# Performance work log

Hardware: AMD Instinct MI355X
Metric: run time of the kernel (lower is better)

Reference implementation:

```python
import jax, jax.numpy as jnp
import numpy as np

HEADS = 16
HEAD_SIZE = 64
INF = 1e12  # bert4keras K.infinity() uses a large finite value


def _rotate_interleaved(x):
    # result[..., 2i] = -x[..., 2i+1]; result[..., 2i+1] = x[..., 2i]
    x2 = jnp.stack([-x[..., 1::2], x[..., ::2]], axis=-1)
    return x2.reshape(x.shape)


def setup_inputs() -> dict:
    key = jax.random.key(0)
    k1, k2 = jax.random.split(key)
    B, N, D = 8, 1024, 1024
    x = jax.random.normal(k1, (B, N, D), dtype=jnp.float32)
    W = jax.random.normal(k2, (D, 2 * HEADS * HEAD_SIZE), dtype=jnp.float32) * (1.0 / np.sqrt(D))
    b = jnp.zeros((2 * HEADS * HEAD_SIZE,), dtype=jnp.float32)
    seq_mask = jnp.ones((B, N), dtype=jnp.float32)
    return {"x": x, "W": W, "b": b, "seq_mask": seq_mask}


def reference(x, W, b, seq_mask):
    B, N, _ = x.shape
    H, d = HEADS, HEAD_SIZE
    proj = x @ W + b                       # [B, N, 2*H*d]
    z = proj.reshape(B, N, H, 2 * d)       # split into heads then stack
    qw, kw = z[..., :d], z[..., d:]        # [B, N, H, d]

    # RoPE (interleaved sin/cos)
    pos = jnp.arange(N, dtype=jnp.float32)
    freqs = jnp.power(10000.0, -2.0 * jnp.arange(d // 2, dtype=jnp.float32) / d)
    ang = pos[:, None] * freqs[None, :]    # [N, d/2]
    cos_pos = jnp.repeat(jnp.cos(ang), 2, axis=-1)[None, :, None, :]  # [1,N,1,d]
    sin_pos = jnp.repeat(jnp.sin(ang), 2, axis=-1)[None, :, None, :]
    qw = qw * cos_pos + _rotate_interleaved(qw) * sin_pos
    kw = kw * cos_pos + _rotate_interleaved(kw) * sin_pos

    logits = jnp.einsum('bmhd,bnhd->bhmn', qw, kw)   # [B, H, N, N]

    # sequence masking on query (axis 2) and key (axis 3)
    logits = logits - (1.0 - seq_mask[:, None, :, None]) * INF
    logits = logits - (1.0 - seq_mask[:, None, None, :]) * INF

    # triangular mask: keep upper triangle including diagonal
    tri = jnp.triu(jnp.ones((N, N), dtype=logits.dtype))
    logits = logits - (1.0 - tri) * INF
    return logits / jnp.sqrt(jnp.float32(d))
```

## Files before the change

### kernel.cpp

```cpp
#include <hip/hip_runtime.h>

typedef __bf16 bf16;
typedef __bf16 bf16x4 __attribute__((ext_vector_type(4)));
typedef __bf16 bf16x8 __attribute__((ext_vector_type(8)));
typedef float f32x4 __attribute__((ext_vector_type(4)));

#define GL(p) ((const __attribute__((address_space(1))) void*)(p))
#define LD(p) ((__attribute__((address_space(3))) void*)(p))

__global__ __launch_bounds__(256) void k_prep(
    const float4* __restrict__ x4, bf16x4* __restrict__ o4,
    const float* __restrict__ W, bf16* __restrict__ Wt,
    float* __restrict__ cost, float* __restrict__ sint)
{
    __shared__ bf16 tile[64][65];
    const int bid = (int)blockIdx.x;
    const int t = threadIdx.x;
    if (bid < 2048) {
        for (int i = bid * 256 + t; i < 2097152; i += 2048 * 256) {
            float4 v = x4[i];
            bf16x4 o;
            o[0] = (bf16)v.x; o[1] = (bf16)v.y; o[2] = (bf16)v.z; o[3] = (bf16)v.w;
            o4[i] = o;
        }
    } else if (bid < 2560) {
        const int wid = bid - 2048;
        const int k0 = (wid & 15) * 64;
        const int n0 = (wid >> 4) * 64;
        const int c = t & 63, r4 = t >> 6;
#pragma unroll
        for (int p = 0; p < 16; ++p) {
            int r = p * 4 + r4;
            tile[r][c] = (bf16)W[(size_t)(k0 + r) * 2048 + n0 + c];
        }
        __syncthreads();
#pragma unroll
        for (int p = 0; p < 16; ++p) {
            int n = p * 4 + r4;
            Wt[(size_t)(n0 + n) * 1024 + k0 + c] = tile[c][n];
        }
    } else {
        int idx = (bid - 2560) * 256 + t;
        int pos = idx >> 5, i = idx & 31;
        float freq = powf(10000.f, -(float)i / 32.f);
        float ang = (float)pos * freq;
        cost[idx] = cosf(ang);
        sint[idx] = sinf(ang);
    }
}

__global__ __launch_bounds__(512) void k_gemm1(
    const bf16* __restrict__ Xb, const bf16* __restrict__ Wt,
    const float* __restrict__ bias,
    const float* __restrict__ cost, const float* __restrict__ sint,
    bf16* __restrict__ Qb, bf16* __restrict__ Kb)
{
    __shared__ bf16 lA[2][256 * 64];
    __shared__ bf16 lB[2][128 * 64];
    const int t = threadIdx.x;
    const int lane = t & 63;
    const int wave = t >> 6;
    const int wr = (wave >> 1) * 64;
    const int wc = (wave & 1) * 64;
    const int bm = (int)blockIdx.x * 256;
    const int bn = (int)blockIdx.y * 128;
    const int rl = lane & 15;
    const int hi = lane >> 4;

    f32x4 acc[4][4] = {};

#define STAGE1(kt, c) do {                                                              \
    _Pragma("unroll")                                                                   \
    for (int p = 0; p < 4; ++p) {                                                       \
        int e = t * 8 + p * 4096;                                                       \
        int row = e >> 6; int g = (e >> 3) & 7;                                         \
        __builtin_amdgcn_global_load_lds(                                               \
            GL(Xb + (size_t)(bm + row) * 1024 + (kt) * 64 + ((g ^ (row & 7)) << 3)),    \
            LD(&lA[c][e]), 16, 0, 0);                                                   \
    }                                                                                   \
    _Pragma("unroll")                                                                   \
    for (int p = 0; p < 2; ++p) {                                                       \
        int e = t * 8 + p * 4096;                                                       \
        int row = e >> 6; int g = (e >> 3) & 7;                                         \
        __builtin_amdgcn_global_load_lds(                                               \
            GL(Wt + (size_t)(bn + row) * 1024 + (kt) * 64 + ((g ^ (row & 7)) << 3)),    \
            LD(&lB[c][e]), 16, 0, 0);                                                   \
    }                                                                                   \
} while (0)

    STAGE1(0, 0);
    STAGE1(1, 1);
    asm volatile("s_waitcnt vmcnt(6)" ::: "memory");
    __builtin_amdgcn_sched_barrier(0);
    __builtin_amdgcn_s_barrier();
    asm volatile("" ::: "memory");

    for (int kt = 0; kt < 16; ++kt) {
        const int cur = kt & 1;
        bf16x8 af[2][4], bfr[2][4];
#pragma unroll
        for (int ks = 0; ks < 2; ++ks) {
#pragma unroll
            for (int m = 0; m < 4; ++m) {
                int R = wr + m * 16 + rl;
                af[ks][m] = *(const bf16x8*)&lA[cur][(R << 6) + (((ks * 4 + hi) ^ (R & 7)) << 3)];
            }
#pragma unroll
            for (int n = 0; n < 4; ++n) {
                int S = wc + n * 16 + rl;
                bfr[ks][n] = *(const bf16x8*)&lB[cur][(S << 6) + (((ks * 4 + hi) ^ (S & 7)) << 3)];
            }
        }
#pragma unroll
        for (int ks = 0; ks < 2; ++ks)
#pragma unroll
            for (int m = 0; m < 4; ++m)
#pragma unroll
                for (int n = 0; n < 4; ++n)
                    acc[m][n] = __builtin_amdgcn_mfma_f32_16x16x32_bf16(af[ks][m], bfr[ks][n], acc[m][n], 0, 0, 0);

        if (kt < 15) {
            __builtin_amdgcn_s_barrier();
            if (kt + 2 < 16) {
                STAGE1(kt + 2, cur);
                asm volatile("s_waitcnt vmcnt(6)" ::: "memory");
            } else {
                asm volatile("s_waitcnt vmcnt(0)" ::: "memory");
            }
            __builtin_amdgcn_sched_barrier(0);
            __builtin_amdgcn_s_barrier();
            asm volatile("" ::: "memory");
        }
    }
#undef STAGE1

#pragma unroll
    for (int m = 0; m < 4; ++m) {
#pragma unroll
        for (int n = 0; n < 4; ++n) {
            int colg = bn + wc + n * 16 + rl;
            float bv = bias[colg];
            int h = colg >> 7;
            int rem = colg & 127;
            int qk = rem >> 6;
            int dcol = rem & 63;
            int fi = dcol >> 1;
            float sgn = (dcol & 1) ? 1.f : -1.f;
            bf16* dstb = qk ? Kb : Qb;
#pragma unroll
            for (int r = 0; r < 4; ++r) {
                int rowg = bm + wr + m * 16 + hi * 4 + r;
                int pos = rowg & 1023, bidx = rowg >> 10;
                float val = acc[m][n][r] + bv;
                float part = __shfl_xor(val, 1);
                float cv = cost[pos * 32 + fi], sv = sint[pos * 32 + fi];
                float outv = val * cv + sgn * part * sv;
                dstb[(((size_t)(bidx * 16 + h)) * 1024 + pos) * 64 + dcol] = (bf16)outv;
            }
        }
    }
}

__global__ __launch_bounds__(256) void k_gemm2(
    const bf16* __restrict__ Qb, const bf16* __restrict__ Kb,
    const float* __restrict__ smask, float* __restrict__ out)
{
    __shared__ bf16 lQ[128 * 64];
    __shared__ bf16 lK[128 * 64];
    const int t = threadIdx.x;
    const int lane = t & 63, wave = t >> 6;
    const int wr = (wave >> 1) * 64, wc = (wave & 1) * 64;
    const int bid = (int)blockIdx.x;
    const int xcd = bid & 7;
    const int idx = bid >> 3;
    const int bh = xcd * 16 + (idx & 15);
    const int tile = idx >> 4;
    const int bm = (tile >> 3) * 128;
    const int bn = (tile & 7) * 128;
    const int b = bh >> 4;
    const int rl = lane & 15, rq = lane >> 4;
    const float NINF = 1.25e11f;

    if (bn + 128 <= bm) {
#pragma unroll
        for (int m = 0; m < 4; ++m) {
#pragma unroll
            for (int r = 0; r < 4; ++r) {
                int mg = bm + wr + m * 16 + rq * 4 + r;
                float mpen = 1.f - smask[b * 1024 + mg];
                size_t rowoff = ((size_t)bh * 1024 + mg) * 1024;
#pragma unroll
                for (int n = 0; n < 4; ++n) {
                    int ng = bn + wc + n * 16 + rl;
                    float npen = 1.f - smask[b * 1024 + ng];
                    out[rowoff + ng] = -(mpen + npen + 1.f) * NINF;
                }
            }
        }
        return;
    }

    const size_t qoff = (size_t)bh * 1024 * 64;
#pragma unroll
    for (int p = 0; p < 4; ++p) {
        int e = t * 8 + p * 2048;
        __builtin_amdgcn_global_load_lds(GL(Qb + qoff + (size_t)bm * 64 + e), LD(&lQ[e]), 16, 0, 0);
        __builtin_amdgcn_global_load_lds(GL(Kb + qoff + (size_t)bn * 64 + e), LD(&lK[e]), 16, 0, 0);
    }
    __syncthreads();

    f32x4 acc[4][4] = {};
    const int kg = rq * 8;
#pragma unroll
    for (int ks = 0; ks < 2; ++ks) {
        bf16x8 af[4], bfr[4];
#pragma unroll
        for (int m = 0; m < 4; ++m) af[m] = *(const bf16x8*)&lQ[(wr + m * 16 + rl) * 64 + ks * 32 + kg];
#pragma unroll
        for (int n = 0; n < 4; ++n) bfr[n] = *(const bf16x8*)&lK[(wc + n * 16 + rl) * 64 + ks * 32 + kg];
#pragma unroll
        for (int m = 0; m < 4; ++m)
#pragma unroll
            for (int n = 0; n < 4; ++n)
                acc[m][n] = __builtin_amdgcn_mfma_f32_16x16x32_bf16(af[m], bfr[n], acc[m][n], 0, 0, 0);
    }

#pragma unroll
    for (int m = 0; m < 4; ++m) {
#pragma unroll
        for (int r = 0; r < 4; ++r) {
            int mg = bm + wr + m * 16 + rq * 4 + r;
            float mpen = 1.f - smask[b * 1024 + mg];
            size_t rowoff = ((size_t)bh * 1024 + mg) * 1024;
#pragma unroll
            for (int n = 0; n < 4; ++n) {
                int ng = bn + wc + n * 16 + rl;
                float npen = 1.f - smask[b * 1024 + ng];
                float pen = mpen + npen + ((ng < mg) ? 1.f : 0.f);
                out[rowoff + ng] = acc[m][n][r] * 0.125f - pen * NINF;
            }
        }
    }
}

extern "C" void kernel_launch(void* const* d_in, const int* in_sizes, int n_in,
                              void* d_out, int out_size, void* d_ws, size_t ws_size,
                              hipStream_t stream) {
    (void)in_sizes; (void)n_in; (void)out_size; (void)ws_size;
    const float* x    = (const float*)d_in[0];
    const float* W    = (const float*)d_in[1];
    const float* bias = (const float*)d_in[2];
    const float* sm   = (const float*)d_in[3];
    float* out = (float*)d_out;

    char* ws = (char*)d_ws;
    size_t o = 0;
    bf16* Xb = (bf16*)(ws + o); o += 8388608ull * 2;
    bf16* Wt = (bf16*)(ws + o); o += 2097152ull * 2;
    bf16* Qb = (bf16*)(ws + o); o += 8388608ull * 2;
    bf16* Kb = (bf16*)(ws + o); o += 8388608ull * 2;
    float* cost = (float*)(ws + o); o += 32768ull * 4;
    float* sint = (float*)(ws + o); o += 32768ull * 4;

    hipLaunchKernelGGL(k_prep, dim3(2688), dim3(256), 0, stream,
                       (const float4*)x, (bf16x4*)Xb, W, Wt, cost, sint);
    hipLaunchKernelGGL(k_gemm1, dim3(32, 16), dim3(512), 0, stream,
                       Xb, Wt, bias, cost, sint, Qb, Kb);
    hipLaunchKernelGGL(k_gemm2, dim3(8192), dim3(256), 0, stream,
                       Qb, Kb, sm, out);
}
```

Measured before the change: 178.2 us.

## Restructure QK kernel into 16-row strips with LDS-staged coalesced nontemporal stores

Replaces the 128x128 tiled QK^T logits kernel with one where each block computes a full 16-row strip across all 1024 key columns. K is streamed in 64-row chunks with an XOR-swizzled LDS layout, and results are staged in a 64KB LDS buffer, then written out as fully coalesced float4 nontemporal stores. Chunks that lie entirely below the diagonal are skipped, and their constant masked values are written directly. The aim is better write efficiency for the 512MB output, which dominates the kernel. The cost is a per-chunk sync loop with little MFMA work, plus large LDS use that limits occupancy.

```diff
diff --git a/kernel.cpp b/kernel.cpp
--- a/kernel.cpp
+++ b/kernel.cpp
@@ -7,6 +7,10 @@
 
 #define GL(p) ((const __attribute__((address_space(1))) void*)(p))
 #define LD(p) ((__attribute__((address_space(3))) void*)(p))
+
+static __device__ __forceinline__ void nt_store4(float* p, f32x4 v) {
+    __builtin_nontemporal_store(v, (f32x4*)p);
+}
 
 __global__ __launch_bounds__(256) void k_prep(
     const float4* __restrict__ x4, bf16x4* __restrict__ o4,
@@ -161,85 +165,88 @@
     }
 }
 
-__global__ __launch_bounds__(256) void k_gemm2(
+__global__ __launch_bounds__(256) void k_qk(
     const bf16* __restrict__ Qb, const bf16* __restrict__ Kb,
     const float* __restrict__ smask, float* __restrict__ out)
 {
-    __shared__ bf16 lQ[128 * 64];
-    __shared__ bf16 lK[128 * 64];
+    __shared__ __align__(16) float obuf[16 * 1024];
+    __shared__ __align__(16) bf16 lK[64 * 64];
+    __shared__ __align__(16) bf16 lQ[16 * 64];
+    __shared__ float npen_l[1024];
+    __shared__ float mpen_l[16];
+
     const int t = threadIdx.x;
-    const int lane = t & 63, wave = t >> 6;
-    const int wr = (wave >> 1) * 64, wc = (wave & 1) * 64;
+    const int lane = t & 63, w = t >> 6;
+    const int rl = lane & 15, hi = lane >> 4;
     const int bid = (int)blockIdx.x;
     const int xcd = bid & 7;
-    const int idx = bid >> 3;
-    const int bh = xcd * 16 + (idx & 15);
-    const int tile = idx >> 4;
-    const int bm = (tile >> 3) * 128;
-    const int bn = (tile & 7) * 128;
+    const int bh = xcd * 16 + ((bid >> 3) & 15);
+    const int strip = bid >> 7;
+    const int bm = strip * 16;
     const int b = bh >> 4;
-    const int rl = lane & 15, rq = lane >> 4;
+    const int cstart = strip >> 2;
     const float NINF = 1.25e11f;
-
-    if (bn + 128 <= bm) {
-#pragma unroll
-        for (int m = 0; m < 4; ++m) {
+    const size_t qoff = (size_t)bh << 16;
+
+    {
+        f32x4 sv = *(const f32x4*)&smask[b * 1024 + t * 4];
+        f32x4 nv;
+#pragma unroll
+        for (int r = 0; r < 4; ++r) nv[r] = 1.f - sv[r];
+        *(f32x4*)&npen_l[t * 4] = nv;
+        if (t < 16) mpen_l[t] = 1.f - smask[b * 1024 + bm + t];
+    }
+
+    if (t < 128) {
+        int row = t >> 3, c16 = t & 7;
+        int se = (row << 6) + ((c16 ^ (row & 7)) << 3);
+        __builtin_amdgcn_global_load_lds(GL(Qb + qoff + (size_t)bm * 64 + se),
+                                         LD(&lQ[t * 8]), 16, 0, 0);
+    }
+
+    for (int c = cstart; c < 16; ++c) {
+#pragma unroll
+        for (int p = 0; p < 2; ++p) {
+            int e = t * 8 + p * 2048;
+            int gr = e >> 3;
+            int row = gr >> 3, c16 = gr & 7;
+            int se = (row << 6) + ((c16 ^ (row & 7)) << 3);
+            __builtin_amdgcn_global_load_lds(GL(Kb + qoff + (size_t)(c * 64) * 64 + se),
+                                             LD(&lK[e]), 16, 0, 0);
+        }
+        __syncthreads();
+        f32x4 acc = {};
+        const int R = w * 16 + rl;
+#pragma unroll
+        for (int ks = 0; ks < 2; ++ks) {
+            bf16x8 a = *(const bf16x8*)&lK[(R << 6) + ((((ks << 2) + hi) ^ (R & 7)) << 3)];
+            bf16x8 q = *(const bf16x8*)&lQ[(rl << 6) + ((((ks << 2) + hi) ^ (rl & 7)) << 3)];
+            acc = __builtin_amdgcn_mfma_f32_16x16x32_bf16(a, q, acc, 0, 0, 0);
+        }
+        int c0b = (c * 64 + w * 16 + hi * 4) * 4;
+        *(f32x4*)((char*)obuf + (rl << 12) + (c0b ^ ((rl & 15) << 4))) = acc;
+        __syncthreads();
+    }
+
+#pragma unroll
+    for (int it = 0; it < 16; ++it) {
+        int gcb = t * 4;
+        int grow = bm + it;
+        float mp = mpen_l[it];
+        f32x4 np = *(const f32x4*)&npen_l[gcb];
+        f32x4 vo;
+        if (gcb >= cstart * 64) {
+            f32x4 v = *(const f32x4*)((char*)obuf + (it << 12) + ((gcb * 4) ^ ((it & 15) << 4)));
 #pragma unroll
             for (int r = 0; r < 4; ++r) {
-                int mg = bm + wr + m * 16 + rq * 4 + r;
-                float mpen = 1.f - smask[b * 1024 + mg];
-                size_t rowoff = ((size_t)bh * 1024 + mg) * 1024;
-#pragma unroll
-                for (int n = 0; n < 4; ++n) {
-                    int ng = bn + wc + n * 16 + rl;
-                    float npen = 1.f - smask[b * 1024 + ng];
-                    out[rowoff + ng] = -(mpen + npen + 1.f) * NINF;
-                }
-            }
-        }
-        return;
-    }
-
-    const size_t qoff = (size_t)bh * 1024 * 64;
-#pragma unroll
-    for (int p = 0; p < 4; ++p) {
-        int e = t * 8 + p * 2048;
-        __builtin_amdgcn_global_load_lds(GL(Qb + qoff + (size_t)bm * 64 + e), LD(&lQ[e]), 16, 0, 0);
-        __builtin_amdgcn_global_load_lds(GL(Kb + qoff + (size_t)bn * 64 + e), LD(&lK[e]), 16, 0, 0);
-    }
-    __syncthreads();
-
-    f32x4 acc[4][4] = {};
-    const int kg = rq * 8;
-#pragma unroll
-    for (int ks = 0; ks < 2; ++ks) {
-        bf16x8 af[4], bfr[4];
-#pragma unroll
-        for (int m = 0; m < 4; ++m) af[m] = *(const bf16x8*)&lQ[(wr + m * 16 + rl) * 64 + ks * 32 + kg];
-#pragma unroll
-        for (int n = 0; n < 4; ++n) bfr[n] = *(const bf16x8*)&lK[(wc + n * 16 + rl) * 64 + ks * 32 + kg];
-#pragma unroll
-        for (int m = 0; m < 4; ++m)
-#pragma unroll
-            for (int n = 0; n < 4; ++n)
-                acc[m][n] = __builtin_amdgcn_mfma_f32_16x16x32_bf16(af[m], bfr[n], acc[m][n], 0, 0, 0);
-    }
-
-#pragma unroll
-    for (int m = 0; m < 4; ++m) {
-#pragma unroll
-        for (int r = 0; r < 4; ++r) {
-            int mg = bm + wr + m * 16 + rq * 4 + r;
-            float mpen = 1.f - smask[b * 1024 + mg];
-            size_t rowoff = ((size_t)bh * 1024 + mg) * 1024;
-#pragma unroll
-            for (int n = 0; n < 4; ++n) {
-                int ng = bn + wc + n * 16 + rl;
-                float npen = 1.f - smask[b * 1024 + ng];
-                float pen = mpen + npen + ((ng < mg) ? 1.f : 0.f);
-                out[rowoff + ng] = acc[m][n][r] * 0.125f - pen * NINF;
-            }
-        }
+                float pen = mp + np[r] + ((gcb + r < grow) ? 1.f : 0.f);
+                vo[r] = v[r] * 0.125f - pen * NINF;
+            }
+        } else {
+#pragma unroll
+            for (int r = 0; r < 4; ++r) vo[r] = -(mp + np[r] + 1.f) * NINF;
+        }
+        nt_store4(&out[((size_t)bh << 20) + ((size_t)grow << 10) + gcb], vo);
     }
 }
 
@@ -266,6 +273,6 @@
                        (const float4*)x, (bf16x4*)Xb, W, Wt, cost, sint);
     hipLaunchKernelGGL(k_gemm1, dim3(32, 16), dim3(512), 0, stream,
                        Xb, Wt, bias, cost, sint, Qb, Kb);
-    hipLaunchKernelGGL(k_gemm2, dim3(8192), dim3(256), 0, stream,
+    hipLaunchKernelGGL(k_qk, dim3(8192), dim3(256), 0, stream,
                        Qb, Kb, sm, out);
 }
```

After: 179.4 us. No clear change (+0.7%).
